# Performance work log

Hardware: AMD Instinct MI355X
Metric: run time of the kernel (lower is better)

The kernel has to match this reference:

```python
import jax, jax.numpy as jnp
import numpy as np

BIG = 1e10  # sentinel for masked-out (padded) points, like pytorch3d's masking


def setup_inputs() -> dict:
    key = jax.random.key(0)
    k1, k2, k3, k4 = jax.random.split(key, 4)
    B, N, M = 16, 4096, 4096
    source_cloud = jax.random.normal(k1, (B, N, 2), dtype=jnp.float32)
    target_cloud = jax.random.normal(k2, (B, M, 2), dtype=jnp.float32)
    source_mask = jax.random.randint(k3, (B,), 0, N)  # lengths1
    target_mask = jax.random.randint(k4, (B,), 0, M)  # lengths2
    return {
        "source_cloud": source_cloud,
        "target_cloud": target_cloud,
        "source_mask": source_mask,
        "target_mask": target_mask,
    }


def reference(source_cloud, target_cloud, source_mask, target_mask):
    # source_cloud: [B, N, 2], target_cloud: [B, M, 2]
    # source_mask/target_mask: int lengths [B] (knn_points lengths1/lengths2)
    B, N, _ = source_cloud.shape
    M = target_cloud.shape[1]

    s2 = jnp.sum(source_cloud * source_cloud, axis=-1)  # [B, N]
    t2 = jnp.sum(target_cloud * target_cloud, axis=-1)  # [B, M]
    # squared pairwise distances [B, N, M]
    d2 = (s2[:, :, None] + t2[:, None, :]
          - 2.0 * jnp.einsum('bnd,bmd->bnm', source_cloud, target_cloud))

    src_valid = jnp.arange(N)[None, :] < source_mask[:, None]  # [B, N]
    tgt_valid = jnp.arange(M)[None, :] < target_mask[:, None]  # [B, M]

    # forward: for each source point, 1-NN over valid target points
    d2_fwd = jnp.where(tgt_valid[:, None, :], d2, BIG)
    min_fwd = jnp.maximum(jnp.min(d2_fwd, axis=-1), 0.0)  # [B, N]
    # backward: for each target point, 1-NN over valid source points
    d2_bwd = jnp.where(src_valid[:, :, None], d2, BIG)
    min_bwd = jnp.maximum(jnp.min(d2_bwd, axis=-2), 0.0)  # [B, M]

    # padded query points get dist 0 (pytorch3d knn_points semantics), then sqrt
    chamfer_forward = jnp.where(src_valid, jnp.sqrt(min_fwd), 0.0)
    chamfer_backward = jnp.where(tgt_valid, jnp.sqrt(min_bwd), 0.0)
    return (chamfer_forward, chamfer_backward)
```

## Files before the change

### kernel.cpp

```cpp
#include <hip/hip_runtime.h>


#define NQ 16
typedef float f2 __attribute__((ext_vector_type(2)));

template<int KA>
__device__ __forceinline__ void scan_queries(
    const float* __restrict__ Qrow,
    const float4* __restrict__ sxy, const f2* __restrict__ sn,
    float* __restrict__ slice, int tid)
{
    float mx[KA], my[KA], s2[KA], best[KA];
    #pragma unroll
    for (int k = 0; k < KA; ++k) {
        const float2 q = ((const float2*)Qrow)[tid + k * 256];
        mx[k] = -2.f * q.x;
        my[k] = -2.f * q.y;
        s2[k] = fmaf(q.x, q.x, q.y * q.y);
        best[k] = 3.0e38f;
    }

    #pragma unroll 4
    for (int j = 0; j < 64; ++j) {
        const float4 xy = sxy[j];
        const f2 xp = f2{xy.x, xy.y};
        const f2 yp = f2{xy.z, xy.w};
        const f2 np = sn[j];
        #pragma unroll
        for (int k = 0; k < KA; ++k) {
            f2 v = xp * mx[k] + np;
            v = yp * my[k] + v;
            best[k] = fminf(best[k], fminf(v.x, v.y));
        }
    }

    #pragma unroll
    for (int k = 0; k < KA; ++k)
        slice[tid + k * 256] = fmaxf(best[k] + s2[k], 0.f);
}

__global__ __launch_bounds__(256, 2) void chamfer_main(
    const float* __restrict__ src, const float* __restrict__ tgt,
    const int* __restrict__ slen, const int* __restrict__ tlen,
    float* __restrict__ part)
{
    __shared__ float4 sh_xy[64];
    __shared__ f2     sh_n[64];

    const int g   = blockIdx.x;
    const int tid = threadIdx.x;

    int row = -1, pc = 0, Lp = 0, acc = 0;
    #pragma unroll
    for (int rr = 0; rr < 32; ++rr) {
        const int L = (rr < 16) ? tlen[rr] : slen[rr - 16];
        const int n = (L + 127) >> 7;
        if (row < 0 && g < acc + n) { row = rr; pc = g - acc; Lp = L; }
        acc += n;
    }
    if (row < 0) return;
    const int dir = row >> 4, b = row & 15;

    const int Lq = dir ? tlen[b] : slen[b];
    const int KACT = (Lq + 255) >> 8;
    if (KACT == 0) return;

    const float* Q = dir ? tgt : src;
    const float* P = dir ? src : tgt;

    if (tid < 64) {
        const int base = pc * 128 + tid * 2;
        const float4 pp = ((const float4*)P)[(b * 4096 + base) >> 1];
        const float n0 = (base + 0 < Lp) ? fmaf(pp.x, pp.x, pp.y * pp.y) : 1e30f;
        const float n1 = (base + 1 < Lp) ? fmaf(pp.z, pp.z, pp.w * pp.w) : 1e30f;
        sh_xy[tid] = make_float4(pp.x, pp.z, pp.y, pp.w);
        sh_n[tid]  = f2{n0, n1};
    }
    __syncthreads();

    const float* Qrow = Q + b * 8192;
    float* slice = part + ((size_t)row * 32 + pc) * 4096;

    switch ((KACT + 3) >> 2) {
        case 1:  scan_queries< 4>(Qrow, sh_xy, sh_n, slice, tid); break;
        case 2:  scan_queries< 8>(Qrow, sh_xy, sh_n, slice, tid); break;
        case 3:  scan_queries<12>(Qrow, sh_xy, sh_n, slice, tid); break;
        default: scan_queries<16>(Qrow, sh_xy, sh_n, slice, tid); break;
    }
}

__global__ __launch_bounds__(128) void chamfer_reduce(
    const float* __restrict__ part,
    const int* __restrict__ slen, const int* __restrict__ tlen,
    float* __restrict__ out)
{
    const int t  = blockIdx.x * 128 + threadIdx.x;
    const int i4 = t * 4;
    const int row = i4 >> 12;
    const int dir = row >> 4, b = row & 15;
    const int i   = i4 & 4095;
    const int Lq = dir ? tlen[b] : slen[b];
    const int Lp = dir ? slen[b] : tlen[b];

    if (i >= Lq) {
        ((float4*)out)[t] = make_float4(0.f, 0.f, 0.f, 0.f);
        return;
    }

    const int nact = (Lp + 127) >> 7;
    float4 best = make_float4(1e10f, 1e10f, 1e10f, 1e10f);
    const float4* p = (const float4*)(part + (size_t)row * 32 * 4096 + i);
    #pragma unroll 4
    for (int s = 0; s < nact; ++s) {
        const float4 v = p[(size_t)s * 1024];
        best.x = fminf(best.x, v.x);
        best.y = fminf(best.y, v.y);
        best.z = fminf(best.z, v.z);
        best.w = fminf(best.w, v.w);
    }
    float4 r;
    r.x = sqrtf(best.x);
    r.y = (i + 1 < Lq) ? sqrtf(best.y) : 0.f;
    r.z = (i + 2 < Lq) ? sqrtf(best.z) : 0.f;
    r.w = (i + 3 < Lq) ? sqrtf(best.w) : 0.f;
    ((float4*)out)[t] = r;
}

extern "C" void kernel_launch(void* const* d_in, const int* in_sizes, int n_in,
                              void* d_out, int out_size, void* d_ws, size_t ws_size,
                              hipStream_t stream) {
    const float* src = (const float*)d_in[0];
    const float* tgt = (const float*)d_in[1];
    const int* slen  = (const int*)d_in[2];
    const int* tlen  = (const int*)d_in[3];
    float* part = (float*)d_ws;

    chamfer_main<<<1024, 256, 0, stream>>>(src, tgt, slen, tlen, part);
    chamfer_reduce<<<256, 128, 0, stream>>>(part, slen, tlen, (float*)d_out);
}
```

Baseline: 84.72 us.

## Replace partial-buffer reduction kernel with atomicMin directly into output

```diff
diff --git a/kernel.cpp b/kernel.cpp
--- a/kernel.cpp
+++ b/kernel.cpp
@@ -8,7 +8,7 @@
 __device__ __forceinline__ void scan_queries(
     const float* __restrict__ Qrow,
     const float4* __restrict__ sxy, const f2* __restrict__ sn,
-    float* __restrict__ slice, int tid)
+    unsigned* __restrict__ orow_u, int tid)
 {
     float mx[KA], my[KA], s2[KA], best[KA];
     #pragma unroll
@@ -35,14 +35,16 @@
     }
 
     #pragma unroll
-    for (int k = 0; k < KA; ++k)
-        slice[tid + k * 256] = fmaxf(best[k] + s2[k], 0.f);
+    for (int k = 0; k < KA; ++k) {
+        const float d = sqrtf(fmaxf(best[k] + s2[k], 0.f));
+        atomicMin(orow_u + tid + k * 256, __float_as_uint(d));
+    }
 }
 
 __global__ __launch_bounds__(256, 2) void chamfer_main(
     const float* __restrict__ src, const float* __restrict__ tgt,
     const int* __restrict__ slen, const int* __restrict__ tlen,
-    float* __restrict__ part)
+    float* __restrict__ out)
 {
     __shared__ float4 sh_xy[64];
     __shared__ f2     sh_n[64];
@@ -58,10 +60,38 @@
         if (row < 0 && g < acc + n) { row = rr; pc = g - acc; Lp = L; }
         acc += n;
     }
-    if (row < 0) return;
+
+    if (row < 0) {
+        const int cr = g - acc;
+        if (cr < 32) {
+            const int dirc = cr >> 4, bc = cr & 15;
+            const int Lpc = dirc ? slen[bc] : tlen[bc];
+            if (Lpc == 0) {
+                const int Lqc = dirc ? tlen[bc] : slen[bc];
+                unsigned* op = (unsigned*)(out + cr * 4096);
+                const unsigned sent = __float_as_uint(sqrtf(1e10f));
+                #pragma unroll
+                for (int k = 0; k < 16; ++k) {
+                    const int q = tid + k * 256;
+                    atomicMin(op + q, (q < Lqc) ? sent : 0u);
+                }
+            }
+        }
+        return;
+    }
     const int dir = row >> 4, b = row & 15;
 
     const int Lq = dir ? tlen[b] : slen[b];
+    unsigned* orow_u = (unsigned*)(out + row * 4096);
+
+    if (pc == 0) {
+        #pragma unroll
+        for (int k = 0; k < 16; ++k) {
+            const int q = tid + k * 256;
+            if (q >= Lq) atomicMin(orow_u + q, 0u);
+        }
+    }
+
     const int KACT = (Lq + 255) >> 8;
     if (KACT == 0) return;
 
@@ -79,51 +109,13 @@
     __syncthreads();
 
     const float* Qrow = Q + b * 8192;
-    float* slice = part + ((size_t)row * 32 + pc) * 4096;
 
     switch ((KACT + 3) >> 2) {
-        case 1:  scan_queries< 4>(Qrow, sh_xy, sh_n, slice, tid); break;
-        case 2:  scan_queries< 8>(Qrow, sh_xy, sh_n, slice, tid); break;
-        case 3:  scan_queries<12>(Qrow, sh_xy, sh_n, slice, tid); break;
-        default: scan_queries<16>(Qrow, sh_xy, sh_n, slice, tid); break;
+        case 1:  scan_queries< 4>(Qrow, sh_xy, sh_n, orow_u, tid); break;
+        case 2:  scan_queries< 8>(Qrow, sh_xy, sh_n, orow_u, tid); break;
+        case 3:  scan_queries<12>(Qrow, sh_xy, sh_n, orow_u, tid); break;
+        default: scan_queries<16>(Qrow, sh_xy, sh_n, orow_u, tid); break;
     }
-}
-
-__global__ __launch_bounds__(128) void chamfer_reduce(
-    const float* __restrict__ part,
-    const int* __restrict__ slen, const int* __restrict__ tlen,
-    float* __restrict__ out)
-{
-    const int t  = blockIdx.x * 128 + threadIdx.x;
-    const int i4 = t * 4;
-    const int row = i4 >> 12;
-    const int dir = row >> 4, b = row & 15;
-    const int i   = i4 & 4095;
-    const int Lq = dir ? tlen[b] : slen[b];
-    const int Lp = dir ? slen[b] : tlen[b];
-
-    if (i >= Lq) {
-        ((float4*)out)[t] = make_float4(0.f, 0.f, 0.f, 0.f);
-        return;
-    }
-
-    const int nact = (Lp + 127) >> 7;
-    float4 best = make_float4(1e10f, 1e10f, 1e10f, 1e10f);
-    const float4* p = (const float4*)(part + (size_t)row * 32 * 4096 + i);
-    #pragma unroll 4
-    for (int s = 0; s < nact; ++s) {
-        const float4 v = p[(size_t)s * 1024];
-        best.x = fminf(best.x, v.x);
-        best.y = fminf(best.y, v.y);
-        best.z = fminf(best.z, v.z);
-        best.w = fminf(best.w, v.w);
-    }
-    float4 r;
-    r.x = sqrtf(best.x);
-    r.y = (i + 1 < Lq) ? sqrtf(best.y) : 0.f;
-    r.z = (i + 2 < Lq) ? sqrtf(best.z) : 0.f;
-    r.w = (i + 3 < Lq) ? sqrtf(best.w) : 0.f;
-    ((float4*)out)[t] = r;
 }
 
 extern "C" void kernel_launch(void* const* d_in, const int* in_sizes, int n_in,
@@ -133,8 +125,8 @@
     const float* tgt = (const float*)d_in[1];
     const int* slen  = (const int*)d_in[2];
     const int* tlen  = (const int*)d_in[3];
-    float* part = (float*)d_ws;
+    (void)d_ws; (void)ws_size;
 
-    chamfer_main<<<1024, 256, 0, stream>>>(src, tgt, slen, tlen, part);
-    chamfer_reduce<<<256, 128, 0, stream>>>(part, slen, tlen, (float*)d_out);
+    hipMemsetAsync(d_out, 0x7F, (size_t)out_size * sizeof(float), stream);
+    chamfer_main<<<1024, 256, 0, stream>>>(src, tgt, slen, tlen, (float*)d_out);
 }
```

New measurement: 79.28 us. 1.07x faster.
